# Performance work log

Hardware: AMD Instinct MI355X
Metric: run time of the kernel (lower is better)

## Reference

```python
import jax, jax.numpy as jnp
import numpy as np

IN_FEATURES = 4096
OUT_FEATURES = 11008
GROUPSIZE = 128
GROUPS = IN_FEATURES // GROUPSIZE  # 32


def setup_inputs() -> dict:
    key = jax.random.key(0)
    k1, k2, k3 = jax.random.split(key, 3)
    input = jax.random.normal(k1, (2, 2048, IN_FEATURES), dtype=jnp.float32)
    # int8-valued weight stored as int32 for portability; values in [-128, 127]
    weight = jax.random.randint(k2, (OUT_FEATURES, IN_FEATURES), -128, 128, dtype=jnp.int32)
    scales = jax.random.uniform(k3, (OUT_FEATURES, GROUPS), dtype=jnp.float32) * 0.02 + 0.001
    return {"input": input, "weight": weight, "scales": scales}


def reference(input, weight, scales):
    # Groupwise dequantization fused into linear, matching the torch module:
    # w_deq = (weight.view(O, G, gs) * scales.view(O, G, 1)).view(O, I)
    O, I = weight.shape
    G = scales.shape[1]
    w = weight.astype(input.dtype).reshape(O, G, I // G)
    w_deq = (w * scales[:, :, None].astype(input.dtype)).reshape(O, I)
    # F.linear: input @ w_deq.T -> [B, S, O]
    return jnp.einsum('bsi,oi->bso', input, w_deq)
```

## Files before the change

### kernel.cpp

```cpp
#include <hip/hip_runtime.h>
#include <hip/hip_bf16.h>
#include <stdint.h>


typedef __bf16 bf16_t;
typedef bf16_t bf16x8 __attribute__((ext_vector_type(8)));
typedef float floatx4 __attribute__((ext_vector_type(4)));

#define M_TOT 4096
#define K_TOT 4096
#define N_TOT 11008
#define NGROUPS 32

__global__ __launch_bounds__(256)
void dequant_w_kernel(const int* __restrict__ W, const float* __restrict__ S,
                      bf16_t* __restrict__ Wq)
{
    const int t = blockIdx.x * 256 + threadIdx.x;
    const int c = t & 511;
    const int n = t >> 9;
    const size_t ibase = (size_t)n * K_TOT + c * 8;
    const int4 w0 = *(const int4*)(W + ibase);
    const int4 w1 = *(const int4*)(W + ibase + 4);
    const float sc = S[n * NGROUPS + (c >> 4)];
    bf16x8 o;
    o[0] = (bf16_t)((float)w0.x * sc);
    o[1] = (bf16_t)((float)w0.y * sc);
    o[2] = (bf16_t)((float)w0.z * sc);
    o[3] = (bf16_t)((float)w0.w * sc);
    o[4] = (bf16_t)((float)w1.x * sc);
    o[5] = (bf16_t)((float)w1.y * sc);
    o[6] = (bf16_t)((float)w1.z * sc);
    o[7] = (bf16_t)((float)w1.w * sc);
    const int c8 = c & 7;
    const int nc = (c8 & 4) | ((c8 & 3) ^ ((n >> 1) & 3));
    const size_t obase = (size_t)n * K_TOT + (size_t)(c >> 3) * 64 + nc * 8;
    *(bf16x8*)(Wq + obase) = o;
}

__global__ __launch_bounds__(256)
void cvt_a_kernel(const float* __restrict__ A, bf16_t* __restrict__ Aq)
{
    const int t = blockIdx.x * 256 + threadIdx.x;
    const int c = t & 511;
    const int m = t >> 9;
    const size_t ibase = (size_t)m * K_TOT + c * 8;
    const float4 a0 = *(const float4*)(A + ibase);
    const float4 a1 = *(const float4*)(A + ibase + 4);
    bf16x8 o;
    o[0] = (bf16_t)a0.x; o[1] = (bf16_t)a0.y; o[2] = (bf16_t)a0.z; o[3] = (bf16_t)a0.w;
    o[4] = (bf16_t)a1.x; o[5] = (bf16_t)a1.y; o[6] = (bf16_t)a1.z; o[7] = (bf16_t)a1.w;
    const int c8 = c & 7;
    const int nc = (c8 & 4) | ((c8 & 3) ^ ((m >> 1) & 3));
    const size_t obase = (size_t)m * K_TOT + (size_t)(c >> 3) * 64 + nc * 8;
    *(bf16x8*)(Aq + obase) = o;
}

__device__ __forceinline__ void gload_lds16(const bf16_t* g, bf16_t* lds)
{
    __builtin_amdgcn_global_load_lds(
        (const __attribute__((address_space(1))) unsigned int*)g,
        (__attribute__((address_space(3))) unsigned int*)lds,
        16, 0, 0);
}

#define GBM 256
#define GBN 256
#define KH  32
#define G_MT (M_TOT / GBM)
#define G_NT (N_TOT / GBN)
#define NKT  (K_TOT / 64)

#define BAR   __builtin_amdgcn_s_barrier()
#define LGKM0 asm volatile("s_waitcnt lgkmcnt(0)" ::: "memory")
#define PRIO1 __builtin_amdgcn_s_setprio(1)
#define PRIO0 __builtin_amdgcn_s_setprio(0)
#define VM(n) asm volatile("s_waitcnt vmcnt(" #n ")" ::: "memory")

#define ST_A(buf, kh, t) do { \
    const bf16_t* s_ = gA + (size_t)(t) * 64 + (kh) * KH; \
    gload_lds16(s_, &shA[buf][kh][sdst]); \
    gload_lds16(s_ + (size_t)128 * K_TOT, &shA[buf][kh][128 * KH + sdst]); \
} while (0)
#define ST_B(buf, kh, t) do { \
    const bf16_t* s_ = gB + (size_t)(t) * 64 + (kh) * KH; \
    gload_lds16(s_, &shB[buf][kh][sdst]); \
    gload_lds16(s_ + (size_t)128 * K_TOT, &shB[buf][kh][128 * KH + sdst]); \
} while (0)

#define LDA(b, ks, mh) do { \
    _Pragma("unroll") \
    for (int i_ = 0; i_ < 4; ++i_) \
        af[i_] = *(const bf16x8*)&shA[b][ks][aBase + ((mh) * 64 + i_ * 16) * KH]; \
} while (0)
#define LDB(b, ks) do { \
    _Pragma("unroll") \
    for (int j_ = 0; j_ < 4; ++j_) \
        bfv[j_] = *(const bf16x8*)&shB[b][ks][bBase + j_ * 16 * KH]; \
} while (0)
#define MM(mh) do { \
    _Pragma("unroll") \
    for (int i_ = 0; i_ < 4; ++i_) \
        _Pragma("unroll") \
        for (int j_ = 0; j_ < 4; ++j_) \
            acc[(mh) * 4 + i_][j_] = __builtin_amdgcn_mfma_f32_16x16x32_bf16( \
                af[i_], bfv[j_], acc[(mh) * 4 + i_][j_], 0, 0, 0); \
} while (0)

#define TILE(b, t, S1, S2, S3, S4, W2, W4) do { \
     \
    LDB(b, 0); LDA(b, 0, 0); S1; \
    BAR; LGKM0; PRIO1; MM(0); PRIO0; BAR; \
     \
    LDA(b, 0, 1); S2; \
    BAR; LGKM0; PRIO1; MM(1); PRIO0; W2; BAR; \
     \
    LDB(b, 1); LDA(b, 1, 0); S3; \
    BAR; LGKM0; PRIO1; MM(0); PRIO0; BAR; \
     \
    LDA(b, 1, 1); S4; \
    BAR; LGKM0; PRIO1; MM(1); PRIO0; W4; BAR; \
} while (0)

__global__ __launch_bounds__(512, 2)
void wq8_gemm_8ph_kernel(const bf16_t* __restrict__ Aq,
                         const bf16_t* __restrict__ Wq,
                         float* __restrict__ C)
{
    __shared__ __align__(16) bf16_t shA[2][2][GBM * KH];
    __shared__ __align__(16) bf16_t shB[2][2][GBN * KH];

    const int bid = blockIdx.x;
    const int u = (bid & 7) * ((G_MT * G_NT) / 8) + (bid >> 3);
    const int mt = u & 15;
    const int nt = u >> 4;
    const int m0 = mt * GBM;
    const int n0 = nt * GBN;

    const int tid = threadIdx.x;
    const int wave = tid >> 6;
    const int lane = tid & 63;
    const int wm = (wave >> 2) * 128;
    const int wn = (wave & 3) * 64;
    const int l15 = lane & 15;
    const int l4 = lane >> 4;
    const int ck = (l4 ^ ((l15 >> 1) & 3)) << 3;

    const int aBase = (wm + l15) * KH + ck;
    const int bBase = (wn + l15) * KH + ck;

    const int srow = wave * 16 + (lane >> 2);
    const int scol = (lane & 3) * 8;
    const bf16_t* gA = Aq + (size_t)(m0 + srow) * K_TOT + scol;
    const bf16_t* gB = Wq + (size_t)(n0 + srow) * K_TOT + scol;
    const int sdst = wave * 16 * KH;

    floatx4 acc[8][4];
#pragma unroll
    for (int i = 0; i < 8; ++i)
#pragma unroll
        for (int j = 0; j < 4; ++j)
            acc[i][j] = (floatx4)0.0f;

    bf16x8 af[4], bfv[4];

    ST_B(0, 0, 0);
    ST_A(0, 0, 0);
    ST_B(0, 1, 0);
    ST_A(0, 1, 0);
    ST_B(1, 0, 1);
    ST_A(1, 0, 1);
    ST_B(1, 1, 1);
    VM(10); BAR;

#pragma unroll 1
    for (int t = 0; t < NKT - 2; t += 2) {
        TILE(0, t,
             ST_A(1, 1, t + 1),
             ST_B(0, 0, t + 2), ST_A(0, 0, t + 2), ST_B(0, 1, t + 2),
             VM(10), VM(10));
        TILE(1, t + 1,
             ST_A(0, 1, t + 2),
             ST_B(1, 0, t + 3), ST_A(1, 0, t + 3), ST_B(1, 1, t + 3),
             VM(10), VM(10));
    }
    TILE(0, 62, ST_A(1, 1, 63), ((void)0), ((void)0), ((void)0), VM(8), VM(4));
    TILE(1, 63, ((void)0), ((void)0), ((void)0), ((void)0), VM(0), ((void)0));

#pragma unroll
    for (int f = 0; f < 8; ++f) {
        const int mb = m0 + wm + (f >> 2) * 64 + (f & 3) * 16 + l4 * 4;
#pragma unroll
        for (int j = 0; j < 4; ++j) {
            const int n = n0 + wn + j * 16 + l15;
#pragma unroll
            for (int r = 0; r < 4; ++r)
                C[(size_t)(mb + r) * N_TOT + n] = acc[f][j][r];
        }
    }
}

#define BM 128
#define BN 128
#define BK 64

__global__ __launch_bounds__(256, 3)
void wq8_gemm_fused_kernel(const float* __restrict__ A,
                           const int*   __restrict__ W,
                           const float* __restrict__ S,
                           float* __restrict__ C)
{
    __shared__ bf16_t As[BM * BK];
    __shared__ bf16_t Bs[BN * BK];

    const int tid = threadIdx.x;
    const int n0 = blockIdx.x * BN;
    const int m0 = blockIdx.y * BM;
    const int wave = tid >> 6;
    const int lane = tid & 63;
    const int wm = (wave >> 1) * 64;
    const int wn = (wave & 1) * 64;
    const int l15 = lane & 15;
    const int l4  = lane >> 4;

    floatx4 acc[4][4];
#pragma unroll
    for (int i = 0; i < 4; ++i)
#pragma unroll
        for (int j = 0; j < 4; ++j)
            acc[i][j] = (floatx4)0.0f;

    const int srow = tid >> 4;
    const int scol = (tid & 15) * 4;
    const int schunk = scol >> 3;
    const int soff = scol & 7;

    for (int k0 = 0; k0 < K_TOT; k0 += BK) {
        const int g = k0 >> 7;
#pragma unroll
        for (int it = 0; it < 8; ++it) {
            const int r = it * 16 + srow;
            const float4 v = *(const float4*)(A + (size_t)(m0 + r) * K_TOT + k0 + scol);
            bf16_t* dst = &As[r * 64 + ((schunk ^ (r & 7)) << 3) + soff];
            dst[0] = (bf16_t)v.x; dst[1] = (bf16_t)v.y;
            dst[2] = (bf16_t)v.z; dst[3] = (bf16_t)v.w;
        }
#pragma unroll
        for (int it = 0; it < 8; ++it) {
            const int r = it * 16 + srow;
            const int4 wv = *(const int4*)(W + (size_t)(n0 + r) * K_TOT + k0 + scol);
            const float sc = S[(size_t)(n0 + r) * NGROUPS + g];
            bf16_t* dst = &Bs[r * 64 + ((schunk ^ (r & 7)) << 3) + soff];
            dst[0] = (bf16_t)((float)wv.x * sc); dst[1] = (bf16_t)((float)wv.y * sc);
            dst[2] = (bf16_t)((float)wv.z * sc); dst[3] = (bf16_t)((float)wv.w * sc);
        }
        __syncthreads();
#pragma unroll
        for (int ks = 0; ks < 2; ++ks) {
            bf16x8 af2[4], bf2[4];
#pragma unroll
            for (int i = 0; i < 4; ++i) {
                const int m = wm + i * 16 + l15;
                const int kc = (l4 + ks * 4) ^ (m & 7);
                af2[i] = *(const bf16x8*)&As[m * 64 + (kc << 3)];
                const int n = wn + i * 16 + l15;
                const int nkc = (l4 + ks * 4) ^ (n & 7);
                bf2[i] = *(const bf16x8*)&Bs[n * 64 + (nkc << 3)];
            }
#pragma unroll
            for (int i = 0; i < 4; ++i)
#pragma unroll
                for (int j = 0; j < 4; ++j)
                    acc[i][j] = __builtin_amdgcn_mfma_f32_16x16x32_bf16(
                        af2[i], bf2[j], acc[i][j], 0, 0, 0);
        }
        __syncthreads();
    }
#pragma unroll
    for (int i = 0; i < 4; ++i) {
        const int mb = m0 + wm + i * 16 + l4 * 4;
#pragma unroll
        for (int j = 0; j < 4; ++j) {
            const int n = n0 + wn + j * 16 + l15;
#pragma unroll
            for (int r = 0; r < 4; ++r)
                C[(size_t)(mb + r) * N_TOT + n] = acc[i][j][r];
        }
    }
}

extern "C" void kernel_launch(void* const* d_in, const int* in_sizes, int n_in,
                              void* d_out, int out_size, void* d_ws, size_t ws_size,
                              hipStream_t stream) {
    const float* A = (const float*)d_in[0];
    const int*   W = (const int*)d_in[1];
    const float* S = (const float*)d_in[2];
    float* C = (float*)d_out;

    const size_t wq_bytes = (size_t)N_TOT * K_TOT * sizeof(bf16_t);
    const size_t aq_bytes = (size_t)M_TOT * K_TOT * sizeof(bf16_t);

    if (ws_size >= wq_bytes + aq_bytes) {
        bf16_t* Wq = (bf16_t*)d_ws;
        bf16_t* Aq = (bf16_t*)((char*)d_ws + wq_bytes);

        dequant_w_kernel<<<(N_TOT * (K_TOT / 8)) / 256, 256, 0, stream>>>(W, S, Wq);
        cvt_a_kernel<<<((size_t)M_TOT * (K_TOT / 8)) / 256, 256, 0, stream>>>(A, Aq);

        wq8_gemm_8ph_kernel<<<dim3(G_MT * G_NT), dim3(512), 0, stream>>>(Aq, Wq, C);
    } else {
        dim3 grid(N_TOT / BN, M_TOT / BM);
        wq8_gemm_fused_kernel<<<grid, dim3(256), 0, stream>>>(A, W, S, C);
    }
}
```

Baseline: 691.2 us.

## Merge prep kernels and switch GEMM to 4-stage LDS ring with one barrier

```diff
diff --git a/kernel.cpp b/kernel.cpp
--- a/kernel.cpp
+++ b/kernel.cpp
@@ -12,48 +12,51 @@
 #define N_TOT 11008
 #define NGROUPS 32
 
+#define W_BLOCKS 22016
+#define A_BLOCKS 8192
+
 __global__ __launch_bounds__(256)
-void dequant_w_kernel(const int* __restrict__ W, const float* __restrict__ S,
-                      bf16_t* __restrict__ Wq)
+void prep_kernel(const int* __restrict__ W, const float* __restrict__ S,
+                 const float* __restrict__ A,
+                 bf16_t* __restrict__ Wq, bf16_t* __restrict__ Aq)
 {
-    const int t = blockIdx.x * 256 + threadIdx.x;
-    const int c = t & 511;
-    const int n = t >> 9;
-    const size_t ibase = (size_t)n * K_TOT + c * 8;
-    const int4 w0 = *(const int4*)(W + ibase);
-    const int4 w1 = *(const int4*)(W + ibase + 4);
-    const float sc = S[n * NGROUPS + (c >> 4)];
-    bf16x8 o;
-    o[0] = (bf16_t)((float)w0.x * sc);
-    o[1] = (bf16_t)((float)w0.y * sc);
-    o[2] = (bf16_t)((float)w0.z * sc);
-    o[3] = (bf16_t)((float)w0.w * sc);
-    o[4] = (bf16_t)((float)w1.x * sc);
-    o[5] = (bf16_t)((float)w1.y * sc);
-    o[6] = (bf16_t)((float)w1.z * sc);
-    o[7] = (bf16_t)((float)w1.w * sc);
-    const int c8 = c & 7;
-    const int nc = (c8 & 4) | ((c8 & 3) ^ ((n >> 1) & 3));
-    const size_t obase = (size_t)n * K_TOT + (size_t)(c >> 3) * 64 + nc * 8;
-    *(bf16x8*)(Wq + obase) = o;
-}
-
-__global__ __launch_bounds__(256)
-void cvt_a_kernel(const float* __restrict__ A, bf16_t* __restrict__ Aq)
-{
-    const int t = blockIdx.x * 256 + threadIdx.x;
-    const int c = t & 511;
-    const int m = t >> 9;
-    const size_t ibase = (size_t)m * K_TOT + c * 8;
-    const float4 a0 = *(const float4*)(A + ibase);
-    const float4 a1 = *(const float4*)(A + ibase + 4);
-    bf16x8 o;
-    o[0] = (bf16_t)a0.x; o[1] = (bf16_t)a0.y; o[2] = (bf16_t)a0.z; o[3] = (bf16_t)a0.w;
-    o[4] = (bf16_t)a1.x; o[5] = (bf16_t)a1.y; o[6] = (bf16_t)a1.z; o[7] = (bf16_t)a1.w;
-    const int c8 = c & 7;
-    const int nc = (c8 & 4) | ((c8 & 3) ^ ((m >> 1) & 3));
-    const size_t obase = (size_t)m * K_TOT + (size_t)(c >> 3) * 64 + nc * 8;
-    *(bf16x8*)(Aq + obase) = o;
+    const int b = blockIdx.x;
+    if (b < W_BLOCKS) {
+        const int t = b * 256 + threadIdx.x;
+        const int c = t & 511;
+        const int n = t >> 9;
+        const size_t ibase = (size_t)n * K_TOT + c * 8;
+        const int4 w0 = *(const int4*)(W + ibase);
+        const int4 w1 = *(const int4*)(W + ibase + 4);
+        const float sc = S[n * NGROUPS + (c >> 4)];
+        bf16x8 o;
+        o[0] = (bf16_t)((float)w0.x * sc);
+        o[1] = (bf16_t)((float)w0.y * sc);
+        o[2] = (bf16_t)((float)w0.z * sc);
+        o[3] = (bf16_t)((float)w0.w * sc);
+        o[4] = (bf16_t)((float)w1.x * sc);
+        o[5] = (bf16_t)((float)w1.y * sc);
+        o[6] = (bf16_t)((float)w1.z * sc);
+        o[7] = (bf16_t)((float)w1.w * sc);
+        const int c8 = c & 7;
+        const int nc = (c8 & 4) | ((c8 & 3) ^ ((n >> 1) & 3));
+        const size_t obase = (size_t)n * K_TOT + (size_t)(c >> 3) * 64 + nc * 8;
+        *(bf16x8*)(Wq + obase) = o;
+    } else {
+        const int t = (b - W_BLOCKS) * 256 + threadIdx.x;
+        const int c = t & 511;
+        const int m = t >> 9;
+        const size_t ibase = (size_t)m * K_TOT + c * 8;
+        const float4 a0 = *(const float4*)(A + ibase);
+        const float4 a1 = *(const float4*)(A + ibase + 4);
+        bf16x8 o;
+        o[0] = (bf16_t)a0.x; o[1] = (bf16_t)a0.y; o[2] = (bf16_t)a0.z; o[3] = (bf16_t)a0.w;
+        o[4] = (bf16_t)a1.x; o[5] = (bf16_t)a1.y; o[6] = (bf16_t)a1.z; o[7] = (bf16_t)a1.w;
+        const int c8 = c & 7;
+        const int nc = (c8 & 4) | ((c8 & 3) ^ ((m >> 1) & 3));
+        const size_t obase = (size_t)m * K_TOT + (size_t)(c >> 3) * 64 + nc * 8;
+        *(bf16x8*)(Aq + obase) = o;
+    }
 }
 
 __device__ __forceinline__ void gload_lds16(const bf16_t* g, bf16_t* lds)
@@ -66,69 +69,63 @@
 
 #define GBM 256
 #define GBN 256
-#define KH  32
+#define KT  32
+#define NKT (K_TOT / KT)
 #define G_MT (M_TOT / GBM)
 #define G_NT (N_TOT / GBN)
-#define NKT  (K_TOT / 64)
-
-#define BAR   __builtin_amdgcn_s_barrier()
-#define LGKM0 asm volatile("s_waitcnt lgkmcnt(0)" ::: "memory")
-#define PRIO1 __builtin_amdgcn_s_setprio(1)
-#define PRIO0 __builtin_amdgcn_s_setprio(0)
-#define VM(n) asm volatile("s_waitcnt vmcnt(" #n ")" ::: "memory")
-
-#define ST_A(buf, kh, t) do { \
-    const bf16_t* s_ = gA + (size_t)(t) * 64 + (kh) * KH; \
-    gload_lds16(s_, &shA[buf][kh][sdst]); \
-    gload_lds16(s_ + (size_t)128 * K_TOT, &shA[buf][kh][128 * KH + sdst]); \
+
+#define BAR     __builtin_amdgcn_s_barrier()
+#define PRIO1   __builtin_amdgcn_s_setprio(1)
+#define PRIO0   __builtin_amdgcn_s_setprio(0)
+#define VM(n)   asm volatile("s_waitcnt vmcnt(" #n ")" ::: "memory")
+#define LGKM(n) asm volatile("s_waitcnt lgkmcnt(" #n ")" ::: "memory")
+
+#define ST4(tb, kk) do { \
+    const bf16_t* sa_ = gA + (size_t)(kk) * KT; \
+    gload_lds16(sa_, &shA[tb][sdst]); \
+    gload_lds16(sa_ + (size_t)128 * K_TOT, &shA[tb][128 * KT + sdst]); \
+    const bf16_t* sb_ = gB + (size_t)(kk) * KT; \
+    gload_lds16(sb_, &shB[tb][sdst]); \
+    gload_lds16(sb_ + (size_t)128 * K_TOT, &shB[tb][128 * KT + sdst]); \
 } while (0)
-#define ST_B(buf, kh, t) do { \
-    const bf16_t* s_ = gB + (size_t)(t) * 64 + (kh) * KH; \
-    gload_lds16(s_, &shB[buf][kh][sdst]); \
-    gload_lds16(s_ + (size_t)128 * K_TOT, &shB[buf][kh][128 * KH + sdst]); \
-} while (0)
-
-#define LDA(b, ks, mh) do { \
-    _Pragma("unroll") \
+
+#define LDB32(b) do { _Pragma("unroll") \
+    for (int j_ = 0; j_ < 4; ++j_) \
+        bfv[j_] = *(const bf16x8*)&shB[b][(wn + j_ * 16 + l15) * KT + ck]; } while (0)
+
+#define LDA32(b, mh, dst) do { _Pragma("unroll") \
     for (int i_ = 0; i_ < 4; ++i_) \
-        af[i_] = *(const bf16x8*)&shA[b][ks][aBase + ((mh) * 64 + i_ * 16) * KH]; \
-} while (0)
-#define LDB(b, ks) do { \
-    _Pragma("unroll") \
-    for (int j_ = 0; j_ < 4; ++j_) \
-        bfv[j_] = *(const bf16x8*)&shB[b][ks][bBase + j_ * 16 * KH]; \
-} while (0)
-#define MM(mh) do { \
-    _Pragma("unroll") \
+        dst[i_] = *(const bf16x8*)&shA[b][(wm + (mh) * 64 + i_ * 16 + l15) * KT + ck]; } while (0)
+
+#define MM32(mh, a_) do { _Pragma("unroll") \
     for (int i_ = 0; i_ < 4; ++i_) \
         _Pragma("unroll") \
         for (int j_ = 0; j_ < 4; ++j_) \
             acc[(mh) * 4 + i_][j_] = __builtin_amdgcn_mfma_f32_16x16x32_bf16( \
-                af[i_], bfv[j_], acc[(mh) * 4 + i_][j_], 0, 0, 0); \
+                a_[i_], bfv[j_], acc[(mh) * 4 + i_][j_], 0, 0, 0); } while (0)
+
+#define TILE32(b, tb, kk, W_) do { \
+    ST4(tb, kk); \
+    LDB32(b); LDA32(b, 0, af); LDA32(b, 1, af2); \
+    LGKM(4); PRIO1; MM32(0, af); PRIO0; \
+    LGKM(0); PRIO1; MM32(1, af2); PRIO0; \
+    W_; BAR; \
 } while (0)
 
-#define TILE(b, t, S1, S2, S3, S4, W2, W4) do { \
-     \
-    LDB(b, 0); LDA(b, 0, 0); S1; \
-    BAR; LGKM0; PRIO1; MM(0); PRIO0; BAR; \
-     \
-    LDA(b, 0, 1); S2; \
-    BAR; LGKM0; PRIO1; MM(1); PRIO0; W2; BAR; \
-     \
-    LDB(b, 1); LDA(b, 1, 0); S3; \
-    BAR; LGKM0; PRIO1; MM(0); PRIO0; BAR; \
-     \
-    LDA(b, 1, 1); S4; \
-    BAR; LGKM0; PRIO1; MM(1); PRIO0; W4; BAR; \
+#define TILE32_NS(b, W_) do { \
+    LDB32(b); LDA32(b, 0, af); LDA32(b, 1, af2); \
+    LGKM(4); PRIO1; MM32(0, af); PRIO0; \
+    LGKM(0); PRIO1; MM32(1, af2); PRIO0; \
+    W_; BAR; \
 } while (0)
 
 __global__ __launch_bounds__(512, 2)
-void wq8_gemm_8ph_kernel(const bf16_t* __restrict__ Aq,
-                         const bf16_t* __restrict__ Wq,
-                         float* __restrict__ C)
+void wq8_gemm_ring_kernel(const bf16_t* __restrict__ Aq,
+                          const bf16_t* __restrict__ Wq,
+                          float* __restrict__ C)
 {
-    __shared__ __align__(16) bf16_t shA[2][2][GBM * KH];
-    __shared__ __align__(16) bf16_t shB[2][2][GBN * KH];
+    __shared__ __align__(16) bf16_t shA[4][GBM * KT];
+    __shared__ __align__(16) bf16_t shB[4][GBN * KT];
 
     const int bid = blockIdx.x;
     const int u = (bid & 7) * ((G_MT * G_NT) / 8) + (bid >> 3);
@@ -146,14 +143,11 @@
     const int l4 = lane >> 4;
     const int ck = (l4 ^ ((l15 >> 1) & 3)) << 3;
 
-    const int aBase = (wm + l15) * KH + ck;
-    const int bBase = (wn + l15) * KH + ck;
-
     const int srow = wave * 16 + (lane >> 2);
     const int scol = (lane & 3) * 8;
     const bf16_t* gA = Aq + (size_t)(m0 + srow) * K_TOT + scol;
     const bf16_t* gB = Wq + (size_t)(n0 + srow) * K_TOT + scol;
-    const int sdst = wave * 16 * KH;
+    const int sdst = wave * 16 * KT;
 
     floatx4 acc[8][4];
 #pragma unroll
@@ -162,30 +156,24 @@
         for (int j = 0; j < 4; ++j)
             acc[i][j] = (floatx4)0.0f;
 
-    bf16x8 af[4], bfv[4];
-
-    ST_B(0, 0, 0);
-    ST_A(0, 0, 0);
-    ST_B(0, 1, 0);
-    ST_A(0, 1, 0);
-    ST_B(1, 0, 1);
-    ST_A(1, 0, 1);
-    ST_B(1, 1, 1);
-    VM(10); BAR;
+    bf16x8 af[4], af2[4], bfv[4];
+
+    ST4(0, 0);
+    ST4(1, 1);
+    ST4(2, 2);
+    VM(8); BAR;
 
 #pragma unroll 1
-    for (int t = 0; t < NKT - 2; t += 2) {
-        TILE(0, t,
-             ST_A(1, 1, t + 1),
-             ST_B(0, 0, t + 2), ST_A(0, 0, t + 2), ST_B(0, 1, t + 2),
-             VM(10), VM(10));
-        TILE(1, t + 1,
-             ST_A(0, 1, t + 2),
-             ST_B(1, 0, t + 3), ST_A(1, 0, t + 3), ST_B(1, 1, t + 3),
-             VM(10), VM(10));
-    }
-    TILE(0, 62, ST_A(1, 1, 63), ((void)0), ((void)0), ((void)0), VM(8), VM(4));
-    TILE(1, 63, ((void)0), ((void)0), ((void)0), ((void)0), VM(0), ((void)0));
+    for (int t = 0; t < NKT - 4; t += 4) {
+        TILE32(0, 3, t + 3, VM(8));
+        TILE32(1, 0, t + 4, VM(8));
+        TILE32(2, 1, t + 5, VM(8));
+        TILE32(3, 2, t + 6, VM(8));
+    }
+    TILE32(0, 3, 127, VM(8));
+    TILE32_NS(1, VM(4));
+    TILE32_NS(2, VM(0));
+    TILE32_NS(3, ((void)0));
 
 #pragma unroll
     for (int f = 0; f < 8; ++f) {
@@ -257,12 +245,12 @@
         __syncthreads();
 #pragma unroll
         for (int ks = 0; ks < 2; ++ks) {
-            bf16x8 af2[4], bf2[4];
+            bf16x8 af2v[4], bf2[4];
 #pragma unroll
             for (int i = 0; i < 4; ++i) {
                 const int m = wm + i * 16 + l15;
                 const int kc = (l4 + ks * 4) ^ (m & 7);
-                af2[i] = *(const bf16x8*)&As[m * 64 + (kc << 3)];
+                af2v[i] = *(const bf16x8*)&As[m * 64 + (kc << 3)];
                 const int n = wn + i * 16 + l15;
                 const int nkc = (l4 + ks * 4) ^ (n & 7);
                 bf2[i] = *(const bf16x8*)&Bs[n * 64 + (nkc << 3)];
@@ -272,7 +260,7 @@
 #pragma unroll
                 for (int j = 0; j < 4; ++j)
                     acc[i][j] = __builtin_amdgcn_mfma_f32_16x16x32_bf16(
-                        af2[i], bf2[j], acc[i][j], 0, 0, 0);
+                        af2v[i], bf2[j], acc[i][j], 0, 0, 0);
         }
         __syncthreads();
     }
@@ -304,10 +292,8 @@
         bf16_t* Wq = (bf16_t*)d_ws;
         bf16_t* Aq = (bf16_t*)((char*)d_ws + wq_bytes);
 
-        dequant_w_kernel<<<(N_TOT * (K_TOT / 8)) / 256, 256, 0, stream>>>(W, S, Wq);
-        cvt_a_kernel<<<((size_t)M_TOT * (K_TOT / 8)) / 256, 256, 0, stream>>>(A, Aq);
-
-        wq8_gemm_8ph_kernel<<<dim3(G_MT * G_NT), dim3(512), 0, stream>>>(Aq, Wq, C);
+        prep_kernel<<<W_BLOCKS + A_BLOCKS, 256, 0, stream>>>(W, S, A, Wq, Aq);
+        wq8_gemm_ring_kernel<<<dim3(G_MT * G_NT), dim3(512), 0, stream>>>(Aq, Wq, C);
     } else {
         dim3 grid(N_TOT / BN, M_TOT / BM);
         wq8_gemm_fused_kernel<<<grid, dim3(256), 0, stream>>>(A, W, S, C);
```

New measurement: 743.1 us. +7.5%, slower.

## Double-buffer LDS fragment registers to overlap ds_reads with MFMA phases

Applied to the files above, without the earlier changes.

```diff
diff --git a/kernel.cpp b/kernel.cpp
--- a/kernel.cpp
+++ b/kernel.cpp
@@ -72,10 +72,11 @@
 #define NKT  (K_TOT / 64)
 
 #define BAR   __builtin_amdgcn_s_barrier()
-#define LGKM0 asm volatile("s_waitcnt lgkmcnt(0)" ::: "memory")
+#define SGB0  __builtin_amdgcn_sched_barrier(0)
 #define PRIO1 __builtin_amdgcn_s_setprio(1)
 #define PRIO0 __builtin_amdgcn_s_setprio(0)
 #define VM(n) asm volatile("s_waitcnt vmcnt(" #n ")" ::: "memory")
+#define NOP   ((void)0)
 
 #define ST_A(buf, kh, t) do { \
     const bf16_t* s_ = gA + (size_t)(t) * 64 + (kh) * KH; \
@@ -88,39 +89,44 @@
     gload_lds16(s_ + (size_t)128 * K_TOT, &shB[buf][kh][128 * KH + sdst]); \
 } while (0)
 
-#define LDA(b, ks, mh) do { \
-    _Pragma("unroll") \
+#define RD_A(dst, b, ks, mh) do { _Pragma("unroll") \
     for (int i_ = 0; i_ < 4; ++i_) \
-        af[i_] = *(const bf16x8*)&shA[b][ks][aBase + ((mh) * 64 + i_ * 16) * KH]; \
-} while (0)
-#define LDB(b, ks) do { \
-    _Pragma("unroll") \
+        dst[i_] = *(const bf16x8*)&shA[b][ks][aBase + ((mh) * 64 + i_ * 16) * KH]; \
+} while (0)
+#define RD_B(dst, b, ks) do { _Pragma("unroll") \
     for (int j_ = 0; j_ < 4; ++j_) \
-        bfv[j_] = *(const bf16x8*)&shB[b][ks][bBase + j_ * 16 * KH]; \
-} while (0)
-#define MM(mh) do { \
-    _Pragma("unroll") \
+        dst[j_] = *(const bf16x8*)&shB[b][ks][bBase + j_ * 16 * KH]; \
+} while (0)
+
+#define MMQ(a_, b_, mh) do { _Pragma("unroll") \
     for (int i_ = 0; i_ < 4; ++i_) \
         _Pragma("unroll") \
         for (int j_ = 0; j_ < 4; ++j_) \
             acc[(mh) * 4 + i_][j_] = __builtin_amdgcn_mfma_f32_16x16x32_bf16( \
-                af[i_], bfv[j_], acc[(mh) * 4 + i_][j_], 0, 0, 0); \
-} while (0)
-
-#define TILE(b, t, S1, S2, S3, S4, W2, W4) do { \
-     \
-    LDB(b, 0); LDA(b, 0, 0); S1; \
-    BAR; LGKM0; PRIO1; MM(0); PRIO0; BAR; \
-     \
-    LDA(b, 0, 1); S2; \
-    BAR; LGKM0; PRIO1; MM(1); PRIO0; W2; BAR; \
-     \
-    LDB(b, 1); LDA(b, 1, 0); S3; \
-    BAR; LGKM0; PRIO1; MM(0); PRIO0; BAR; \
-     \
-    LDA(b, 1, 1); S4; \
-    BAR; LGKM0; PRIO1; MM(1); PRIO0; W4; BAR; \
-} while (0)
+                a_[i_], b_[j_], acc[(mh) * 4 + i_], 0, 0, 0); \
+} while (0)
+#undef MMQ
+#define MMQ(a_, b_, mh) do { _Pragma("unroll") \
+    for (int i_ = 0; i_ < 4; ++i_) \
+        _Pragma("unroll") \
+        for (int j_ = 0; j_ < 4; ++j_) \
+            acc[(mh) * 4 + i_][j_] = __builtin_amdgcn_mfma_f32_16x16x32_bf16( \
+                a_[i_], b_[j_], acc[(mh) * 4 + i_][j_], 0, 0, 0); \
+} while (0)
+
+#define P1(b, S_, W_) do { \
+    RD_A(af1, b, 0, 1); S_; SGB0; BAR; \
+    PRIO1; MMQ(af0, bf0, 0); PRIO0; W_; BAR; } while (0)
+#define P2(b, S_, W_) do { \
+    RD_B(bf1, b, 1); RD_A(af0, b, 1, 0); S_; SGB0; BAR; \
+    PRIO1; MMQ(af1, bf0, 1); PRIO0; W_; BAR; } while (0)
+#define P3(b, S_, W_) do { \
+    RD_A(af1, b, 1, 1); S_; SGB0; BAR; \
+    PRIO1; MMQ(af0, bf1, 0); PRIO0; W_; BAR; } while (0)
+#define P4(bn, S_, W_) do { \
+    RD_B(bf0, bn, 0); RD_A(af0, bn, 0, 0); S_; SGB0; BAR; \
+    PRIO1; MMQ(af1, bf1, 1); PRIO0; W_; BAR; } while (0)
+#define P4F do { SGB0; BAR; PRIO1; MMQ(af1, bf1, 1); PRIO0; } while (0)
 
 __global__ __launch_bounds__(512, 2)
 void wq8_gemm_8ph_kernel(const bf16_t* __restrict__ Aq,
@@ -162,7 +168,7 @@
         for (int j = 0; j < 4; ++j)
             acc[i][j] = (floatx4)0.0f;
 
-    bf16x8 af[4], bfv[4];
+    bf16x8 af0[4], af1[4], bf0[4], bf1[4];
 
     ST_B(0, 0, 0);
     ST_A(0, 0, 0);
@@ -172,20 +178,29 @@
     ST_A(1, 0, 1);
     ST_B(1, 1, 1);
     VM(10); BAR;
+    RD_B(bf0, 0, 0);
+    RD_A(af0, 0, 0, 0);
+    SGB0;
 
 #pragma unroll 1
     for (int t = 0; t < NKT - 2; t += 2) {
-        TILE(0, t,
-             ST_A(1, 1, t + 1),
-             ST_B(0, 0, t + 2), ST_A(0, 0, t + 2), ST_B(0, 1, t + 2),
-             VM(10), VM(10));
-        TILE(1, t + 1,
-             ST_A(0, 1, t + 2),
-             ST_B(1, 0, t + 3), ST_A(1, 0, t + 3), ST_B(1, 1, t + 3),
-             VM(10), VM(10));
-    }
-    TILE(0, 62, ST_A(1, 1, 63), ((void)0), ((void)0), ((void)0), VM(8), VM(4));
-    TILE(1, 63, ((void)0), ((void)0), ((void)0), ((void)0), VM(0), ((void)0));
+        P1(0, ST_A(1, 1, t + 1), VM(8));
+        P2(0, ST_B(0, 0, t + 2), NOP);
+        P3(0, ST_A(0, 0, t + 2), VM(8));
+        P4(1, ST_B(0, 1, t + 2), NOP);
+        P1(1, ST_A(0, 1, t + 2), VM(8));
+        P2(1, ST_B(1, 0, t + 3), NOP);
+        P3(1, ST_A(1, 0, t + 3), VM(8));
+        P4(0, ST_B(1, 1, t + 3), NOP);
+    }
+    P1(0, ST_A(1, 1, 63), VM(8));
+    P2(0, NOP, NOP);
+    P3(0, NOP, VM(4));
+    P4(1, NOP, NOP);
+    P1(1, NOP, VM(0));
+    P2(1, NOP, NOP);
+    P3(1, NOP, NOP);
+    P4F;
 
 #pragma unroll
     for (int f = 0; f < 8; ++f) {
@@ -257,12 +272,12 @@
         __syncthreads();
 #pragma unroll
         for (int ks = 0; ks < 2; ++ks) {
-            bf16x8 af2[4], bf2[4];
+            bf16x8 af2v[4], bf2[4];
 #pragma unroll
             for (int i = 0; i < 4; ++i) {
                 const int m = wm + i * 16 + l15;
                 const int kc = (l4 + ks * 4) ^ (m & 7);
-                af2[i] = *(const bf16x8*)&As[m * 64 + (kc << 3)];
+                af2v[i] = *(const bf16x8*)&As[m * 64 + (kc << 3)];
                 const int n = wn + i * 16 + l15;
                 const int nkc = (l4 + ks * 4) ^ (n & 7);
                 bf2[i] = *(const bf16x8*)&Bs[n * 64 + (nkc << 3)];
@@ -272,7 +287,7 @@
 #pragma unroll
                 for (int j = 0; j < 4; ++j)
                     acc[i][j] = __builtin_amdgcn_mfma_f32_16x16x32_bf16(
-                        af2[i], bf2[j], acc[i][j], 0, 0, 0);
+                        af2v[i], bf2[j], acc[i][j], 0, 0, 0);
         }
         __syncthreads();
     }
```

Measured after the change: 720.6 us. +4.2%, slower.

## Use nontemporal loads/stores in prep kernels and epilogue, drop explicit lgkmcnt waits

Applied to the files above, without the earlier changes.

```diff
diff --git a/kernel.cpp b/kernel.cpp
--- a/kernel.cpp
+++ b/kernel.cpp
@@ -6,6 +6,8 @@
 typedef __bf16 bf16_t;
 typedef bf16_t bf16x8 __attribute__((ext_vector_type(8)));
 typedef float floatx4 __attribute__((ext_vector_type(4)));
+typedef int   intx4  __attribute__((ext_vector_type(4)));
+typedef float fltx4  __attribute__((ext_vector_type(4)));
 
 #define M_TOT 4096
 #define K_TOT 4096
@@ -20,18 +22,19 @@
     const int c = t & 511;
     const int n = t >> 9;
     const size_t ibase = (size_t)n * K_TOT + c * 8;
-    const int4 w0 = *(const int4*)(W + ibase);
-    const int4 w1 = *(const int4*)(W + ibase + 4);
+    const intx4* wp = (const intx4*)(W + ibase);
+    const intx4 w0 = __builtin_nontemporal_load(wp);
+    const intx4 w1 = __builtin_nontemporal_load(wp + 1);
     const float sc = S[n * NGROUPS + (c >> 4)];
     bf16x8 o;
-    o[0] = (bf16_t)((float)w0.x * sc);
-    o[1] = (bf16_t)((float)w0.y * sc);
-    o[2] = (bf16_t)((float)w0.z * sc);
-    o[3] = (bf16_t)((float)w0.w * sc);
-    o[4] = (bf16_t)((float)w1.x * sc);
-    o[5] = (bf16_t)((float)w1.y * sc);
-    o[6] = (bf16_t)((float)w1.z * sc);
-    o[7] = (bf16_t)((float)w1.w * sc);
+    o[0] = (bf16_t)((float)w0[0] * sc);
+    o[1] = (bf16_t)((float)w0[1] * sc);
+    o[2] = (bf16_t)((float)w0[2] * sc);
+    o[3] = (bf16_t)((float)w0[3] * sc);
+    o[4] = (bf16_t)((float)w1[0] * sc);
+    o[5] = (bf16_t)((float)w1[1] * sc);
+    o[6] = (bf16_t)((float)w1[2] * sc);
+    o[7] = (bf16_t)((float)w1[3] * sc);
     const int c8 = c & 7;
     const int nc = (c8 & 4) | ((c8 & 3) ^ ((n >> 1) & 3));
     const size_t obase = (size_t)n * K_TOT + (size_t)(c >> 3) * 64 + nc * 8;
@@ -45,11 +48,12 @@
     const int c = t & 511;
     const int m = t >> 9;
     const size_t ibase = (size_t)m * K_TOT + c * 8;
-    const float4 a0 = *(const float4*)(A + ibase);
-    const float4 a1 = *(const float4*)(A + ibase + 4);
+    const fltx4* ap = (const fltx4*)(A + ibase);
+    const fltx4 a0 = __builtin_nontemporal_load(ap);
+    const fltx4 a1 = __builtin_nontemporal_load(ap + 1);
     bf16x8 o;
-    o[0] = (bf16_t)a0.x; o[1] = (bf16_t)a0.y; o[2] = (bf16_t)a0.z; o[3] = (bf16_t)a0.w;
-    o[4] = (bf16_t)a1.x; o[5] = (bf16_t)a1.y; o[6] = (bf16_t)a1.z; o[7] = (bf16_t)a1.w;
+    o[0] = (bf16_t)a0[0]; o[1] = (bf16_t)a0[1]; o[2] = (bf16_t)a0[2]; o[3] = (bf16_t)a0[3];
+    o[4] = (bf16_t)a1[0]; o[5] = (bf16_t)a1[1]; o[6] = (bf16_t)a1[2]; o[7] = (bf16_t)a1[3];
     const int c8 = c & 7;
     const int nc = (c8 & 4) | ((c8 & 3) ^ ((m >> 1) & 3));
     const size_t obase = (size_t)m * K_TOT + (size_t)(c >> 3) * 64 + nc * 8;
@@ -72,7 +76,6 @@
 #define NKT  (K_TOT / 64)
 
 #define BAR   __builtin_amdgcn_s_barrier()
-#define LGKM0 asm volatile("s_waitcnt lgkmcnt(0)" ::: "memory")
 #define PRIO1 __builtin_amdgcn_s_setprio(1)
 #define PRIO0 __builtin_amdgcn_s_setprio(0)
 #define VM(n) asm volatile("s_waitcnt vmcnt(" #n ")" ::: "memory")
@@ -110,16 +113,16 @@
 #define TILE(b, t, S1, S2, S3, S4, W2, W4) do { \
      \
     LDB(b, 0); LDA(b, 0, 0); S1; \
-    BAR; LGKM0; PRIO1; MM(0); PRIO0; BAR; \
+    BAR; PRIO1; MM(0); PRIO0; BAR; \
      \
     LDA(b, 0, 1); S2; \
-    BAR; LGKM0; PRIO1; MM(1); PRIO0; W2; BAR; \
+    BAR; PRIO1; MM(1); PRIO0; W2; BAR; \
      \
     LDB(b, 1); LDA(b, 1, 0); S3; \
-    BAR; LGKM0; PRIO1; MM(0); PRIO0; BAR; \
+    BAR; PRIO1; MM(0); PRIO0; BAR; \
      \
     LDA(b, 1, 1); S4; \
-    BAR; LGKM0; PRIO1; MM(1); PRIO0; W4; BAR; \
+    BAR; PRIO1; MM(1); PRIO0; W4; BAR; \
 } while (0)
 
 __global__ __launch_bounds__(512, 2)
@@ -195,7 +198,8 @@
             const int n = n0 + wn + j * 16 + l15;
 #pragma unroll
             for (int r = 0; r < 4; ++r)
-                C[(size_t)(mb + r) * N_TOT + n] = acc[f][j][r];
+                __builtin_nontemporal_store(acc[f][j][r],
+                                            &C[(size_t)(mb + r) * N_TOT + n]);
         }
     }
 }
@@ -257,12 +261,12 @@
         __syncthreads();
 #pragma unroll
         for (int ks = 0; ks < 2; ++ks) {
-            bf16x8 af2[4], bf2[4];
+            bf16x8 af2v[4], bf2[4];
 #pragma unroll
             for (int i = 0; i < 4; ++i) {
                 const int m = wm + i * 16 + l15;
                 const int kc = (l4 + ks * 4) ^ (m & 7);
-                af2[i] = *(const bf16x8*)&As[m * 64 + (kc << 3)];
+                af2v[i] = *(const bf16x8*)&As[m * 64 + (kc << 3)];
                 const int n = wn + i * 16 + l15;
                 const int nkc = (l4 + ks * 4) ^ (n & 7);
                 bf2[i] = *(const bf16x8*)&Bs[n * 64 + (nkc << 3)];
@@ -272,7 +276,7 @@
 #pragma unroll
                 for (int j = 0; j < 4; ++j)
                     acc[i][j] = __builtin_amdgcn_mfma_f32_16x16x32_bf16(
-                        af2[i], bf2[j], acc[i][j], 0, 0, 0);
+                        af2v[i], bf2[j], acc[i][j], 0, 0, 0);
         }
         __syncthreads();
     }
```

After: 653.8 us. 5.4% less time.
